# Optimization experiments

Measured on AMD Instinct MI355X. Metric: run time of the kernel, lower is better.

## Reference

```python
import jax, jax.numpy as jnp
import numpy as np

N = 20000        # nodes per type
E = 320000       # edges per type (avg degree 16)
H = 8            # heads
F0 = 128         # initial feature dim
F_UNI = 256      # n_unified
F_OUT = 64       # n_units per layer
N_USER = 20000   # shape_ret[0]
N_CLASSES = 2


def setup_inputs() -> dict:
    key = jax.random.key(0)
    ks = jax.random.split(key, 32)
    nrm = lambda k, s: jax.random.normal(k, s, dtype=jnp.float32) * 0.05
    inp = {
        "hemb0": nrm(ks[0], (N, F0)),
        "hemb1": nrm(ks[1], (N, F0)),
        "W0": nrm(ks[2], (F0, F_UNI)),
        "W1": nrm(ks[3], (F0, F_UNI)),
    }
    i = 4
    for t in range(2):
        for l, fin in enumerate([F_UNI, H * F_OUT]):
            inp[f"g{t}l{l}_w"] = nrm(ks[i], (H, fin, F_OUT)); i += 1
            inp[f"g{t}l{l}_asrc"] = nrm(ks[i], (H, F_OUT)); i += 1
            inp[f"g{t}l{l}_atrg"] = nrm(ks[i], (H, F_OUT)); i += 1
    inp["aw1"] = nrm(ks[i], (F_UNI, F_OUT)); i += 1
    inp["aw2"] = nrm(ks[i], (F_OUT, F_OUT)); i += 1
    inp["am"] = nrm(ks[i], (F_OUT,)); i += 1
    inp["fc_w"] = nrm(ks[i], (F_OUT * 3, N_CLASSES)); i += 1
    inp["fc_b"] = jnp.zeros((N_CLASSES,), jnp.float32); i += 1
    inp["edge0"] = jax.random.randint(ks[i], (2, E), 0, N, dtype=jnp.int32); i += 1
    inp["edge1"] = jax.random.randint(ks[i], (2, E), 0, N, dtype=jnp.int32)
    return inp


def spgat(h, src, trg, w, asrc, atrg):
    """Sparse GAT layer: h [N,f_in], edge list src/trg [E] -> [N,H,f_out]."""
    n = h.shape[0]
    hp = jnp.einsum('nf,hfo->hno', h, w)              # [H,N,O]
    s = jnp.einsum('hno,ho->nh', hp, asrc)            # [N,H]
    t = jnp.einsum('hno,ho->nh', hp, atrg)            # [N,H]
    e = jax.nn.leaky_relu(s[src] + t[trg], negative_slope=0.2)  # [E,H]
    ex = jnp.exp(e - jnp.max(e))                      # global max shift (as in source)
    denom = jax.ops.segment_sum(ex, trg, num_segments=n)[trg] + 1e-16
    alpha = ex / denom                                # [E,H]
    msg = jnp.transpose(hp, (1, 0, 2))[src] * alpha[:, :, None]  # [E,H,O]
    return jax.ops.segment_sum(msg, trg, num_segments=n)         # [N,H,O]


def reference(hemb0, hemb1, W0, W1,
              g0l0_w, g0l0_asrc, g0l0_atrg, g0l1_w, g0l1_asrc, g0l1_atrg,
              g1l0_w, g1l0_asrc, g1l0_atrg, g1l1_w, g1l1_asrc, g1l1_atrg,
              aw1, aw2, am, fc_w, fc_b, edge0, edge1):
    trans0 = hemb0 @ W0                                # [N,F_UNI]
    trans1 = hemb1 @ W1
    stacks = [
        (trans0, edge0, (g0l0_w, g0l0_asrc, g0l0_atrg), (g0l1_w, g0l1_asrc, g0l1_atrg)),
        (trans1, edge1, (g1l0_w, g1l0_asrc, g1l0_atrg), (g1l1_w, g1l1_asrc, g1l1_atrg)),
    ]
    heter = []
    for trans, edge, p0, p1 in stacks:
        src, trg = edge[0], edge[1]
        x = spgat(trans, src, trg, *p0)                # [N,H,F_OUT]
        x = jax.nn.elu(x.reshape(N, -1))               # [N,H*F_OUT]
        x = spgat(x, src, trg, *p1).mean(axis=1)       # [N,F_OUT]
        heter.append(x[:N_USER][:, None, :])
    type_aware = jnp.concatenate(heter, axis=1)        # [N_USER, 2, F_OUT]
    # faithful to source: feature = trans_emb[0] where trans_emb is the LAST
    # type's transformed embedding -> row 0, shape [F_UNI], broadcast over nodes
    feature = trans1[0]
    q = jnp.tanh(feature @ aw1 + type_aware @ aw2)     # [N_USER,2,F_OUT]
    beta = jax.nn.softmax(q @ am, axis=-1)             # [N_USER,2]
    fusion = jnp.einsum('nr,nrd->nd', beta, type_aware)[:, None, :]
    ret = jnp.concatenate([type_aware, fusion], axis=1).reshape(N_USER, -1)
    return jax.nn.log_softmax(ret @ fc_w + fc_b, axis=-1)   # [N_USER, 2]
```

## Files before the change

### kernel.cpp

```cpp
#include <hip/hip_runtime.h>
#include <hip/hip_bf16.h>


typedef __hip_bfloat16 bf16;
typedef __attribute__((ext_vector_type(8))) short short8;
typedef __attribute__((ext_vector_type(4))) float f32x4;

__device__ __forceinline__ float bf2f(bf16 v) { return __bfloat162float(v); }
__device__ __forceinline__ float ldin(const void* p, long i, int f32) {
  return f32 ? ((const float*)p)[i] : bf2f(((const bf16*)p)[i]);
}
__device__ __forceinline__ short f2bfbits(float f) {
  bf16 h = __float2bfloat16(f);
  return *reinterpret_cast<short*>(&h);
}
__device__ __forceinline__ float bfbits2f(short b) {
  unsigned u = ((unsigned)(unsigned short)b) << 16;
  return __uint_as_float(u);
}

struct GArg {
  const void* A[2];
  const void* B[2];
  bf16* C[2];
  const void* sa[2];
  const void* sb[2];
  float* sv[2];
  float* tv[2];
};

struct AArg {
  const bf16* hp[2];
  const float* sv[2];
  const float* tv[2];
  const int* rp[2];
  const int* col[2];
  void* out[2];
};

__global__ __launch_bounds__(64) void detect_kernel(const void* __restrict__ x,
                                                    int* __restrict__ flag) {
  int tid = threadIdx.x;
  float m = 0.f;
  for (int i = tid; i < 2048; i += 64) {
    float v = fabsf(bf2f(((const bf16*)x)[i]));
    if (!(v <= 1e3f)) v = 1e9f;
    m = fmaxf(m, v);
  }
#pragma unroll
  for (int off = 32; off; off >>= 1) m = fmaxf(m, __shfl_xor(m, off));
  if (tid == 0) flag[0] = (m > 1e3f) ? 1 : 0;
}

__global__ __launch_bounds__(256) void tr_kernel(const bf16* __restrict__ wg,
                                                 bf16* __restrict__ wgT,
                                                 const void* __restrict__ gw1a,
                                                 const void* __restrict__ gw1b,
                                                 bf16* __restrict__ bt1,
                                                 const int* __restrict__ flag) {
  const int f32 = flag[0];
  long i = (long)blockIdx.x * 256 + threadIdx.x;
  const long nW = 2L * 512 * 128;
  const long nB = 2L * 512 * 512;
  if (i < nW) {
    int t = (int)(i >> 16);
    long r = i & 65535;
    int c = (int)(r >> 7), k = (int)(r & 127);
    wgT[i] = wg[(long)t * 65536 + (long)k * 512 + c];
  } else if (i < nW + nB) {
    long r = i - nW;
    int t = (int)(r >> 18);
    long q = r & 262143;
    int c = (int)(q >> 9), k = (int)(q & 511);
    const void* g = t ? gw1b : gw1a;
    float v = ldin(g, ((long)(c >> 6) * 512 + k) * 64 + (c & 63), f32);
    bt1[r] = __float2bfloat16(v);
  }
}

#define GBM 128
#define GBN 64
#define GBK 64

__device__ __forceinline__ int swz(int row, int kbyte) {
  return row * 128 + (kbyte ^ ((row & 7) << 4));
}

__global__ __launch_bounds__(256) void gemm_mfma(GArg g, int amode, int bmode,
                                                 int M, int K, int Nc,
                                                 const int* __restrict__ flag) {
  __shared__ bf16 As[GBM * GBK];
  __shared__ bf16 Bs[GBN * GBK];
  const int z = blockIdx.z;
  const void* __restrict__ A = g.A[z];
  const void* __restrict__ B = g.B[z];
  bf16* __restrict__ C = g.C[z];
  const void* stasrc = g.sa[z];
  const void* statrg = g.sb[z];
  float* svp = g.sv[z];
  float* tvp = g.tv[z];
  const int f32 = flag[0];
  const int af32 = (amode == 1) ? f32 : 0;
  const int bf32 = (bmode == 2 || bmode == 3) ? 0 : f32;

  const int nx = gridDim.x >> 3;
  const int d = blockIdx.x;
  const int fullC = (gridDim.x >> 6) << 6;
  int x, y;
  if (d < fullC) {
    x = (d & 7) + ((d >> 6) << 3);
    y = (d >> 3) & 7;
  } else {
    int l = d - fullC;
    int xbase = fullC >> 3;
    int nrem = nx - xbase;
    x = xbase + l % nrem;
    y = l / nrem;
  }
  const int m0 = x * GBM;
  const int n0 = y * GBN;
  const int tid = threadIdx.x;
  const int lane = tid & 63;
  const int wrow = (tid >> 6) * 32;

  f32x4 acc[2][4];
#pragma unroll
  for (int m = 0; m < 2; m++)
#pragma unroll
    for (int n = 0; n < 4; n++)
#pragma unroll
      for (int r = 0; r < 4; r++) acc[m][n][r] = 0.f;

  for (int kt = 0; kt < K; kt += GBK) {
#pragma unroll
    for (int j = 0; j < 4; j++) {
      int idx = tid + j * 256;
      int row = idx >> 3;
      int ks = idx & 7;
      int gm = m0 + row;
      short8 v;
#pragma unroll
      for (int e = 0; e < 8; e++) v[e] = 0;
      if (gm < M) {
        long base = (long)gm * K + kt + ks * 8;
        if (!af32) {
          v = *(const short8*)((const bf16*)A + base);
        } else {
          const float* Af = (const float*)A + base;
          float4 x0 = *(const float4*)Af;
          float4 x1 = *(const float4*)(Af + 4);
          v[0] = f2bfbits(x0.x); v[1] = f2bfbits(x0.y);
          v[2] = f2bfbits(x0.z); v[3] = f2bfbits(x0.w);
          v[4] = f2bfbits(x1.x); v[5] = f2bfbits(x1.y);
          v[6] = f2bfbits(x1.z); v[7] = f2bfbits(x1.w);
        }
      }
      *(short8*)((char*)As + swz(row, ks * 16)) = v;
    }
    if (bmode == 3) {
      const bf16* BT = (const bf16*)B;
#pragma unroll
      for (int j = 0; j < 2; j++) {
        int idx = tid + j * 256;
        int c = idx >> 3;
        int ks = idx & 7;
        short8 v = *(const short8*)(BT + (long)(n0 + c) * K + kt + ks * 8);
        *(short8*)((char*)Bs + swz(c, ks * 16)) = v;
      }
    } else {
      int n = tid & 63;
      int ks0 = tid >> 6;
#pragma unroll
      for (int jj = 0; jj < 2; jj++) {
        int ks = ks0 + jj * 4;
        int k = kt + ks * 8;
        int col = n0 + n;
        long base;
        int cstr;
        if (bmode == 1) { base = ((long)(col >> 6) * K + k) * 64 + (col & 63); cstr = 64; }
        else { base = (long)k * Nc + col; cstr = Nc; }
        short8 v;
        if (bf32) {
          const float* Bf = (const float*)B;
#pragma unroll
          for (int e = 0; e < 8; e++) v[e] = f2bfbits(Bf[base + (long)e * cstr]);
        } else {
          const bf16* Bh = (const bf16*)B;
#pragma unroll
          for (int e = 0; e < 8; e++) v[e] = *(const short*)&Bh[base + (long)e * cstr];
        }
        *(short8*)((char*)Bs + swz(n, ks * 16)) = v;
      }
    }
    __syncthreads();
#pragma unroll
    for (int kh = 0; kh < 2; kh++) {
      int klane = kh * 64 + ((lane >> 4) << 4);
      short8 af[2], bfr[4];
#pragma unroll
      for (int m = 0; m < 2; m++) {
        int row = wrow + m * 16 + (lane & 15);
        af[m] = *(const short8*)((const char*)As + swz(row, klane));
      }
#pragma unroll
      for (int n = 0; n < 4; n++) {
        int col = n * 16 + (lane & 15);
        bfr[n] = *(const short8*)((const char*)Bs + swz(col, klane));
      }
#pragma unroll
      for (int m = 0; m < 2; m++)
#pragma unroll
        for (int n = 0; n < 4; n++)
          acc[m][n] = __builtin_amdgcn_mfma_f32_16x16x32_bf16(af[m], bfr[n], acc[m][n], 0, 0, 0);
    }
    __syncthreads();
  }
  if (svp) {
    const int h = y;
    const int cl = lane & 15;
    float av[4], bv[4];
#pragma unroll
    for (int n = 0; n < 4; n++) {
      av[n] = ldin(stasrc, h * 64 + n * 16 + cl, f32);
      bv[n] = ldin(statrg, h * 64 + n * 16 + cl, f32);
    }
#pragma unroll
    for (int m = 0; m < 2; m++) {
#pragma unroll
      for (int r = 0; r < 4; r++) {
        float s = 0.f, t = 0.f;
#pragma unroll
        for (int n = 0; n < 4; n++) {
          s += acc[m][n][r] * av[n];
          t += acc[m][n][r] * bv[n];
        }
#pragma unroll
        for (int off = 1; off <= 8; off <<= 1) {
          s += __shfl_xor(s, off);
          t += __shfl_xor(t, off);
        }
        int row = m0 + wrow + m * 16 + ((lane >> 4) << 2) + r;
        if (cl == 0 && row < M) {
          svp[(long)row * 8 + h] = s;
          tvp[(long)row * 8 + h] = t;
        }
      }
    }
  }
#pragma unroll
  for (int m = 0; m < 2; m++) {
#pragma unroll
    for (int r = 0; r < 4; r++) {
      int row = m0 + wrow + m * 16 + ((lane >> 4) << 2) + r;
      if (row < M) {
#pragma unroll
        for (int n = 0; n < 4; n++) {
          int col = n0 + n * 16 + (lane & 15);
          C[(long)row * Nc + col] = __float2bfloat16(acc[m][n][r]);
        }
      }
    }
  }
}

#define FKBM 64

__device__ __forceinline__ int swz256(int row, int kbyte) {
  return row * 256 + (kbyte ^ ((row & 7) << 4));
}

__global__ __launch_bounds__(256) void gemm_fullk(GArg g, int M,
                                                  const int* __restrict__ flag) {
  __shared__ bf16 As[FKBM * 128];
  __shared__ bf16 Bs[64 * 128];
  const int z = blockIdx.z;
  const void* __restrict__ A = g.A[z];
  const bf16* __restrict__ BT = (const bf16*)g.B[z];
  bf16* __restrict__ C = g.C[z];
  const void* stasrc = g.sa[z];
  const void* statrg = g.sb[z];
  float* svp = g.sv[z];
  float* tvp = g.tv[z];
  const int f32 = flag[0];
  const int m0 = blockIdx.x * FKBM;
  const int tid = threadIdx.x;
  const int lane = tid & 63;
  const int wrow = (tid >> 6) * 16;

#pragma unroll
  for (int j = 0; j < 4; j++) {
    int idx = tid + j * 256;
    int row = idx >> 4;
    int ks = idx & 15;
    int gm = m0 + row;
    short8 v;
#pragma unroll
    for (int e = 0; e < 8; e++) v[e] = 0;
    if (gm < M) {
      long base = (long)gm * 128 + ks * 8;
      if (!f32) {
        v = *(const short8*)((const bf16*)A + base);
      } else {
        const float* Af = (const float*)A + base;
        float4 x0 = *(const float4*)Af;
        float4 x1 = *(const float4*)(Af + 4);
        v[0] = f2bfbits(x0.x); v[1] = f2bfbits(x0.y);
        v[2] = f2bfbits(x0.z); v[3] = f2bfbits(x0.w);
        v[4] = f2bfbits(x1.x); v[5] = f2bfbits(x1.y);
        v[6] = f2bfbits(x1.z); v[7] = f2bfbits(x1.w);
      }
    }
    *(short8*)((char*)As + swz256(row, ks * 16)) = v;
  }

  for (int p = 0; p < 8; p++) {
#pragma unroll
    for (int j = 0; j < 4; j++) {
      int idx = tid + j * 256;
      int c = idx >> 4;
      int ks = idx & 15;
      short8 v = *(const short8*)(BT + (long)(p * 64 + c) * 128 + ks * 8);
      *(short8*)((char*)Bs + swz256(c, ks * 16)) = v;
    }
    __syncthreads();
    f32x4 acc[4];
#pragma unroll
    for (int n = 0; n < 4; n++)
#pragma unroll
      for (int r = 0; r < 4; r++) acc[n][r] = 0.f;
#pragma unroll
    for (int kb = 0; kb < 4; kb++) {
      int klane = kb * 64 + ((lane >> 4) << 4);
      short8 af = *(const short8*)((const char*)As + swz256(wrow + (lane & 15), klane));
      short8 bfr[4];
#pragma unroll
      for (int n = 0; n < 4; n++)
        bfr[n] = *(const short8*)((const char*)Bs + swz256(n * 16 + (lane & 15), klane));
#pragma unroll
      for (int n = 0; n < 4; n++)
        acc[n] = __builtin_amdgcn_mfma_f32_16x16x32_bf16(af, bfr[n], acc[n], 0, 0, 0);
    }
    {
      const int cl = lane & 15;
      float av[4], bv[4];
#pragma unroll
      for (int n = 0; n < 4; n++) {
        av[n] = ldin(stasrc, p * 64 + n * 16 + cl, f32);
        bv[n] = ldin(statrg, p * 64 + n * 16 + cl, f32);
      }
#pragma unroll
      for (int r = 0; r < 4; r++) {
        float s = 0.f, t = 0.f;
#pragma unroll
        for (int n = 0; n < 4; n++) {
          s += acc[n][r] * av[n];
          t += acc[n][r] * bv[n];
        }
#pragma unroll
        for (int off = 1; off <= 8; off <<= 1) {
          s += __shfl_xor(s, off);
          t += __shfl_xor(t, off);
        }
        int row = m0 + wrow + ((lane >> 4) << 2) + r;
        if (cl == 0 && row < M) {
          svp[(long)row * 8 + p] = s;
          tvp[(long)row * 8 + p] = t;
        }
      }
    }
#pragma unroll
    for (int r = 0; r < 4; r++) {
      int row = m0 + wrow + ((lane >> 4) << 2) + r;
      if (row < M) {
#pragma unroll
        for (int n = 0; n < 4; n++) {
          int col = p * 64 + n * 16 + (lane & 15);
          C[(long)row * 512 + col] = __float2bfloat16(acc[n][r]);
        }
      }
    }
    __syncthreads();
  }
}

__global__ void hist2_kernel(const int* __restrict__ trg0, const int* __restrict__ trg1,
                             int* __restrict__ deg, int E, int N) {
  int e = blockIdx.x * 256 + threadIdx.x;
  if (e < E) atomicAdd(&deg[trg0[e]], 1);
  else if (e < 2 * E) atomicAdd(&deg[N + trg1[e - E]], 1);
}

__global__ __launch_bounds__(1024) void scan_kernel(const int* __restrict__ degb,
                                                    int* __restrict__ rpb,
                                                    int* __restrict__ filb, int N) {
  const int* deg = degb + (long)blockIdx.x * N;
  int* row_ptr = rpb + (long)blockIdx.x * (N + 1);
  int* fil = filb + (long)blockIdx.x * N;
  __shared__ int sums[1024];
  int tid = threadIdx.x;
  int chunk = (N + 1023) >> 10;
  int start = tid * chunk;
  int end = start + chunk;
  if (start > N) start = N;
  if (end > N) end = N;
  int s = 0;
  for (int i = start; i < end; i++) s += deg[i];
  sums[tid] = s;
  __syncthreads();
  for (int off = 1; off < 1024; off <<= 1) {
    int add = (tid >= off) ? sums[tid - off] : 0;
    __syncthreads();
    sums[tid] += add;
    __syncthreads();
  }
  int run = (tid > 0) ? sums[tid - 1] : 0;
  for (int i = start; i < end; i++) {
    row_ptr[i] = run;
    fil[i] = run;
    run += deg[i];
  }
  if (tid == 0) row_ptr[N] = sums[1023];
}

__global__ void fill2_kernel(const int* __restrict__ src0, const int* __restrict__ trg0,
                             const int* __restrict__ src1, const int* __restrict__ trg1,
                             int* __restrict__ filb, int* __restrict__ colb, int E, int N) {
  int e = blockIdx.x * 256 + threadIdx.x;
  if (e < E) {
    int t = trg0[e];
    int pos = atomicAdd(&filb[t], 1);
    colb[pos] = src0[e];
  } else if (e < 2 * E) {
    int ee = e - E;
    int t = trg1[ee];
    int pos = atomicAdd(&filb[N + t], 1);
    colb[E + pos] = src1[ee];
  }
}

__device__ __forceinline__ float exleaky(float v) {
  v = v > 0.f ? v : 0.2f * v;
  return __expf(v);
}

__global__ __launch_bounds__(256) void aggregate(AArg aa, int N, int mode) {
  const int ty = blockIdx.y;
  const bf16* __restrict__ hpb = aa.hp[ty];
  const float* __restrict__ svb = aa.sv[ty];
  const float* __restrict__ tvb = aa.tv[ty];
  const int* __restrict__ rp = aa.rp[ty];
  const int* __restrict__ colv = aa.col[ty];
  void* __restrict__ outp = aa.out[ty];
  const int wid = threadIdx.x >> 6;
  const int lane = threadIdx.x & 63;
  const int n = blockIdx.x * 4 + wid;
  if (n >= N) return;
  const int start = rp[n];
  const int deg = rp[n + 1] - start;
  const int h = lane >> 3;
  const float tvh = tvb[(long)n * 8 + h];
  const bf16* __restrict__ hpc = hpb + lane * 8;

  float acc[8] = {0.f, 0.f, 0.f, 0.f, 0.f, 0.f, 0.f, 0.f};
  float den = 1e-16f;

#define AG_LOAD(EB, V0, V1, V2, V3, Q0, Q1, Q2, Q3)                 \
  {                                                                 \
    int t0 = __shfl(mysrc, (EB) + 0), t1 = __shfl(mysrc, (EB) + 1); \
    int t2 = __shfl(mysrc, (EB) + 2), t3 = __shfl(mysrc, (EB) + 3); \
    V0 = *(const short8*)(hpc + (long)t0 * 512);                    \
    V1 = *(const short8*)(hpc + (long)t1 * 512);                    \
    V2 = *(const short8*)(hpc + (long)t2 * 512);                    \
    V3 = *(const short8*)(hpc + (long)t3 * 512);                    \
    Q0 = svb[(long)t0 * 8 + h];                                     \
    Q1 = svb[(long)t1 * 8 + h];                                     \
    Q2 = svb[(long)t2 * 8 + h];                                     \
    Q3 = svb[(long)t3 * 8 + h];                                     \
  }
#define AG_ACC(V0, V1, V2, V3, Q0, Q1, Q2, Q3)                      \
  {                                                                 \
    float a0 = exleaky(Q0 + tvh), a1 = exleaky(Q1 + tvh);           \
    float a2 = exleaky(Q2 + tvh), a3 = exleaky(Q3 + tvh);           \
    den += a0 + a1 + a2 + a3;                                       \
    _Pragma("unroll")                                               \
    for (int j = 0; j < 8; j++)                                     \
      acc[j] += a0 * bfbits2f(V0[j]) + a1 * bfbits2f(V1[j]) +       \
                a2 * bfbits2f(V2[j]) + a3 * bfbits2f(V3[j]);        \
  }

  for (int base = 0; base < deg; base += 64) {
    int cnt = deg - base;
    if (cnt > 64) cnt = 64;
    int mysrc = (lane < cnt) ? colv[start + base + lane] : 0;
    int nfull = cnt & ~3;
    if (nfull) {
      short8 v0, v1, v2, v3;
      float q0, q1, q2, q3;
      AG_LOAD(0, v0, v1, v2, v3, q0, q1, q2, q3);
      for (int e = 4; e < nfull; e += 4) {
        short8 w0 = v0, w1 = v1, w2 = v2, w3 = v3;
        float p0 = q0, p1 = q1, p2 = q2, p3 = q3;
        AG_LOAD(e, v0, v1, v2, v3, q0, q1, q2, q3);
        AG_ACC(w0, w1, w2, w3, p0, p1, p2, p3);
      }
      AG_ACC(v0, v1, v2, v3, q0, q1, q2, q3);
    }
    for (int e = nfull; e < cnt; e++) {
      int s0 = __shfl(mysrc, e);
      short8 v = *(const short8*)(hpc + (long)s0 * 512);
      float a = exleaky(svb[(long)s0 * 8 + h] + tvh);
      den += a;
#pragma unroll
      for (int j = 0; j < 8; j++) acc[j] += a * bfbits2f(v[j]);
    }
  }

  const float dinv = 1.f / den;
  if (mode == 0) {
    short8 o8;
#pragma unroll
    for (int j = 0; j < 8; j++) {
      float s = acc[j] * dinv;
      float ev = s > 0.f ? s : expm1f(s);
      o8[j] = f2bfbits(ev);
    }
    *(short8*)((bf16*)outp + (long)n * 512 + lane * 8) = o8;
  } else {
    float r[8];
#pragma unroll
    for (int j = 0; j < 8; j++) r[j] = acc[j] * dinv;
#pragma unroll
    for (int m = 8; m <= 32; m <<= 1)
#pragma unroll
      for (int j = 0; j < 8; j++) r[j] += __shfl_xor(r[j], m);
    if (lane < 8) {
      float* o = (float*)outp + (long)n * 128 + lane * 8;
#pragma unroll
      for (int j = 0; j < 8; j++) o[j] = r[j] * 0.125f;
    }
  }
}

__global__ __launch_bounds__(256) void favec2_kernel(const void* __restrict__ hemb1,
                                                     const void* __restrict__ W1,
                                                     const void* __restrict__ aw1,
                                                     float* __restrict__ favec,
                                                     const int* __restrict__ flag) {
  const int f32 = flag[0];
  __shared__ float s_h[128];
  __shared__ float s_r[256];
  __shared__ float part[4][64];
  const int tid = threadIdx.x;
  if (tid < 128) s_h[tid] = ldin(hemb1, tid, f32);
  __syncthreads();
  float r = 0.f;
  for (int i = 0; i < 128; i++) r += s_h[i] * ldin(W1, (long)i * 256 + tid, f32);
  s_r[tid] = r;
  __syncthreads();
  const int o = tid & 63;
  const int wv = tid >> 6;
  float acc = 0.f;
#pragma unroll
  for (int kk = 0; kk < 64; kk++) {
    int k = wv * 64 + kk;
    acc += s_r[k] * ldin(aw1, (long)k * 64 + o, f32);
  }
  part[wv][o] = acc;
  __syncthreads();
  if (tid < 64) favec[o] = part[0][o] + part[1][o] + part[2][o] + part[3][o];
}

#define FN 16
__global__ __launch_bounds__(256) void final_kernel(const float* __restrict__ ta,
                                                    const float* __restrict__ favec,
                                                    const void* __restrict__ aw2,
                                                    const void* __restrict__ am,
                                                    const void* __restrict__ fcw,
                                                    const void* __restrict__ fcb,
                                                    void* __restrict__ out, int N,
                                                    const int* __restrict__ flag) {
  const int f32 = flag[0];
  __shared__ float s_w[64 * 64];
  __shared__ float s_fc[384];
  __shared__ float s_misc[130];
  __shared__ float s_ta[FN * 128];
  const int tid = threadIdx.x;
  const int n0 = blockIdx.x * FN;
  for (int i = tid; i < 4096; i += 256) s_w[i] = ldin(aw2, i, f32);
  for (int i = tid; i < 384; i += 256) s_fc[i] = ldin(fcw, i, f32);
  if (tid < 64) s_misc[tid] = favec[tid];
  else if (tid < 128) s_misc[tid] = ldin(am, tid - 64, f32);
  else if (tid < 130) s_misc[tid] = ldin(fcb, tid - 128, f32);
  for (int idx = tid; idx < FN * 128; idx += 256) {
    int ni = idx >> 7;
    int j = idx & 127;
    int k = j >> 1, r = j & 1;
    int n = n0 + ni;
    s_ta[idx] = (n < N) ? ta[(long)n * 128 + r * 64 + k] : 0.f;
  }
  __syncthreads();
  const int o = tid & 63;
  const int wv = tid >> 6;
#pragma unroll
  for (int ni4 = 0; ni4 < 4; ni4++) {
    const int ni = wv * 4 + ni4;
    const int n = n0 + ni;
    if (n >= N) continue;
    const float* tb = &s_ta[ni * 128];
    float acc0 = s_misc[o], acc1 = acc0;
#pragma unroll 8
    for (int k = 0; k < 64; k++) {
      float2 t2 = *(const float2*)(tb + k * 2);
      float w = s_w[k * 64 + o];
      acc0 += t2.x * w;
      acc1 += t2.y * w;
    }
    float ta0 = tb[o * 2];
    float ta1 = tb[o * 2 + 1];
    float amv = s_misc[64 + o];
    float p0 = tanhf(acc0) * amv;
    float p1 = tanhf(acc1) * amv;
#pragma unroll
    for (int off = 32; off > 0; off >>= 1) {
      p0 += __shfl_xor(p0, off);
      p1 += __shfl_xor(p1, off);
    }
    float mx = fmaxf(p0, p1);
    float e0 = __expf(p0 - mx), e1 = __expf(p1 - mx);
    float b0 = e0 / (e0 + e1), b1 = e1 / (e0 + e1);
    float fus = b0 * ta0 + b1 * ta1;
    float l0 = ta0 * s_fc[o * 2 + 0] + ta1 * s_fc[(64 + o) * 2 + 0] + fus * s_fc[(128 + o) * 2 + 0];
    float l1 = ta0 * s_fc[o * 2 + 1] + ta1 * s_fc[(64 + o) * 2 + 1] + fus * s_fc[(128 + o) * 2 + 1];
#pragma unroll
    for (int off = 32; off > 0; off >>= 1) {
      l0 += __shfl_xor(l0, off);
      l1 += __shfl_xor(l1, off);
    }
    if (o == 0) {
      l0 += s_misc[128];
      l1 += s_misc[129];
      float m2 = fmaxf(l0, l1);
      float lse = m2 + logf(__expf(l0 - m2) + __expf(l1 - m2));
      if (f32) {
        ((float*)out)[n * 2 + 0] = l0 - lse;
        ((float*)out)[n * 2 + 1] = l1 - lse;
      } else {
        ((bf16*)out)[n * 2 + 0] = __float2bfloat16(l0 - lse);
        ((bf16*)out)[n * 2 + 1] = __float2bfloat16(l1 - lse);
      }
    }
  }
}

extern "C" void kernel_launch(void* const* d_in, const int* in_sizes, int n_in,
                              void* d_out, int out_size, void* d_ws, size_t ws_size,
                              hipStream_t stream) {
  constexpr int N = 20000, E = 320000, H = 8, F0 = 128, FU = 256, FO = 64;
  const void* hemb[2] = {d_in[0], d_in[1]};
  const void* W[2] = {d_in[2], d_in[3]};
  const void* gw[2][2] = {{d_in[4], d_in[7]}, {d_in[10], d_in[13]}};
  const void* gasrc[2][2] = {{d_in[5], d_in[8]}, {d_in[11], d_in[14]}};
  const void* gatrg[2][2] = {{d_in[6], d_in[9]}, {d_in[12], d_in[15]}};
  const void* aw1 = d_in[16];
  const void* aw2 = d_in[17];
  const void* am = d_in[18];
  const void* fcw = d_in[19];
  const void* fcb = d_in[20];
  const int* edge[2] = {(const int*)d_in[21], (const int*)d_in[22]};

  const size_t szWg = (size_t)F0 * 512 * 2;
  const size_t szWgT = szWg;
  const size_t szBT1 = (size_t)512 * 512 * 2;
  const size_t szHp = (size_t)N * 512 * 2;
  const size_t szSv = (size_t)N * 8 * 4;
  size_t need = 0;
  auto addsz = [&](size_t b) { need += (b + 255) & ~(size_t)255; };
  addsz(4);
  addsz(szWg * 2); addsz(szWgT * 2); addsz(szBT1 * 2);
  addsz(szHp * 2); addsz(szHp * 2);
  addsz(szSv * 2); addsz(szSv * 2);
  addsz((size_t)N * 128 * 4); addsz(256);
  addsz((size_t)2 * N * 4); addsz((size_t)2 * (N + 1) * 4);
  addsz((size_t)2 * N * 4); addsz((size_t)2 * E * 4);
  const bool batched = (ws_size >= need + 4096);
  const int TB = batched ? 2 : 1;

  char* p = (char*)d_ws;
  auto alloc = [&](size_t bytes) -> void* {
    void* r = (void*)p;
    p += (bytes + 255) & ~(size_t)255;
    return r;
  };
  int* flag = (int*)alloc(4);
  bf16* wg = (bf16*)alloc(szWg * 2);
  bf16* wgT = (bf16*)alloc(szWgT * 2);
  bf16* bt1 = (bf16*)alloc(szBT1 * 2);
  bf16* hp = (bf16*)alloc(szHp * TB);
  bf16* xbuf = (bf16*)alloc(szHp * TB);
  float* sv = (float*)alloc(szSv * TB);
  float* tv = (float*)alloc(szSv * TB);
  float* ta = (float*)alloc((size_t)N * 128 * 4);
  float* favec = (float*)alloc(256);
  int* degb = (int*)alloc((size_t)2 * N * 4);
  int* rpb = (int*)alloc((size_t)2 * (N + 1) * 4);
  int* filb = (int*)alloc((size_t)2 * N * 4);
  int* colb = (int*)alloc((size_t)2 * E * 4);

  detect_kernel<<<1, 64, 0, stream>>>(hemb[0], flag);

  hipMemsetAsync(degb, 0, (size_t)2 * N * 4, stream);
  hist2_kernel<<<(2 * E + 255) / 256, 256, 0, stream>>>(edge[0] + E, edge[1] + E, degb, E, N);
  scan_kernel<<<2, 1024, 0, stream>>>(degb, rpb, filb, N);
  fill2_kernel<<<(2 * E + 255) / 256, 256, 0, stream>>>(edge[0], edge[0] + E,
                                                        edge[1], edge[1] + E, filb, colb, E, N);

  favec2_kernel<<<1, 256, 0, stream>>>(hemb[1], W[1], aw1, favec, flag);

  {
    GArg gW{};
    for (int i = 0; i < 2; i++) {
      gW.A[i] = W[i]; gW.B[i] = gw[i][0]; gW.C[i] = wg + (size_t)i * F0 * 512;
      gW.sa[i] = nullptr; gW.sb[i] = nullptr; gW.sv[i] = nullptr; gW.tv[i] = nullptr;
    }
    gemm_mfma<<<dim3(8, 1, 2), 256, 0, stream>>>(gW, 1, 1, F0, FU, H * FO, flag);
  }

  tr_kernel<<<2560, 256, 0, stream>>>(wg, wgT, gw[0][1], gw[1][1], bt1, flag);

  const int gmx = (N + GBM - 1) / GBM;
  const int gfk = (N + FKBM - 1) / FKBM;
  const int npass = batched ? 1 : 2;
  const int TC = batched ? 2 : 1;

  auto hpP = [&](int b) { return hp + (size_t)b * N * 512; };
  auto xbufP = [&](int b) { return xbuf + (size_t)b * N * 512; };
  auto svP = [&](int b) { return sv + (size_t)b * N * 8; };
  auto tvP = [&](int b) { return tv + (size_t)b * N * 8; };

  for (int pass = 0; pass < npass; pass++) {
    int types[2] = {batched ? 0 : pass, batched ? 1 : pass};
    int bufs[2] = {0, batched ? 1 : 0};

    GArg g1{};
    for (int i = 0; i < TC; i++) {
      int t = types[i], b = bufs[i];
      g1.A[i] = hemb[t]; g1.B[i] = wgT + (size_t)t * 512 * 128; g1.C[i] = hpP(b);
      g1.sa[i] = gasrc[t][0]; g1.sb[i] = gatrg[t][0]; g1.sv[i] = svP(b); g1.tv[i] = tvP(b);
    }
    gemm_fullk<<<dim3(gfk, 1, TC), 256, 0, stream>>>(g1, N, flag);

    AArg a0{};
    for (int i = 0; i < TC; i++) {
      int t = types[i], b = bufs[i];
      a0.hp[i] = hpP(b); a0.sv[i] = svP(b); a0.tv[i] = tvP(b);
      a0.rp[i] = rpb + (size_t)t * (N + 1); a0.col[i] = colb + (size_t)t * E;
      a0.out[i] = xbufP(b);
    }
    aggregate<<<dim3((N + 3) / 4, TC), 256, 0, stream>>>(a0, N, 0);

    GArg g2{};
    for (int i = 0; i < TC; i++) {
      int t = types[i], b = bufs[i];
      g2.A[i] = xbufP(b); g2.B[i] = bt1 + (size_t)t * 512 * 512; g2.C[i] = hpP(b);
      g2.sa[i] = gasrc[t][1]; g2.sb[i] = gatrg[t][1]; g2.sv[i] = svP(b); g2.tv[i] = tvP(b);
    }
    gemm_mfma<<<dim3(gmx * 8, 1, TC), 256, 0, stream>>>(g2, 0, 3, N, H * FO, H * FO, flag);

    AArg a1{};
    for (int i = 0; i < TC; i++) {
      int t = types[i], b = bufs[i];
      a1.hp[i] = hpP(b); a1.sv[i] = svP(b); a1.tv[i] = tvP(b);
      a1.rp[i] = rpb + (size_t)t * (N + 1); a1.col[i] = colb + (size_t)t * E;
      a1.out[i] = ta + (size_t)t * FO;
    }
    aggregate<<<dim3((N + 3) / 4, TC), 256, 0, stream>>>(a1, N, 1);
  }

  final_kernel<<<(N + FN - 1) / FN, 256, 0, stream>>>(ta, favec, aw2, am, fcw, fcb, d_out, N, flag);
}
```

Before: 529.8 us.

## Split aggregation across heads and edges per wave with shuffle reduction

The aggregation kernel now launches one wave per (node, head) rather than one wave per node, with the head taken from a new grid dimension. The 64 lanes form 8 groups that each walk every eighth edge, then combine partial sums with xor-shuffles. The mean over heads in mode 1 becomes atomic adds into a buffer that is zeroed beforehand. This raises parallelism and spreads the per-node edge walk across lanes, at the cost of 8x more waves, gathers of only 128 bytes per edge, repeated index loads per head, and float atomics.

After: 1.118 ms. +111.1%, slower.

```diff
diff --git a/kernel.cpp b/kernel.cpp
--- a/kernel.cpp
+++ b/kernel.cpp
@@ -443,100 +443,83 @@
   return __expf(v);
 }
 
-__global__ __launch_bounds__(256) void aggregate(AArg aa, int N, int mode) {
-  const int ty = blockIdx.y;
+__global__ __launch_bounds__(256) void aggregate_h(AArg aa, int N, int mode) {
+  const int ty = blockIdx.z;
   const bf16* __restrict__ hpb = aa.hp[ty];
   const float* __restrict__ svb = aa.sv[ty];
   const float* __restrict__ tvb = aa.tv[ty];
   const int* __restrict__ rp = aa.rp[ty];
   const int* __restrict__ colv = aa.col[ty];
   void* __restrict__ outp = aa.out[ty];
+  const int h = blockIdx.y;
   const int wid = threadIdx.x >> 6;
   const int lane = threadIdx.x & 63;
   const int n = blockIdx.x * 4 + wid;
   if (n >= N) return;
   const int start = rp[n];
   const int deg = rp[n + 1] - start;
-  const int h = lane >> 3;
+  const int grp = lane >> 3;
+  const int il = lane & 7;
   const float tvh = tvb[(long)n * 8 + h];
-  const bf16* __restrict__ hpc = hpb + lane * 8;
+  const bf16* __restrict__ hpc = hpb + h * 64 + il * 8;
 
   float acc[8] = {0.f, 0.f, 0.f, 0.f, 0.f, 0.f, 0.f, 0.f};
-  float den = 1e-16f;
-
-#define AG_LOAD(EB, V0, V1, V2, V3, Q0, Q1, Q2, Q3)                 \
-  {                                                                 \
-    int t0 = __shfl(mysrc, (EB) + 0), t1 = __shfl(mysrc, (EB) + 1); \
-    int t2 = __shfl(mysrc, (EB) + 2), t3 = __shfl(mysrc, (EB) + 3); \
-    V0 = *(const short8*)(hpc + (long)t0 * 512);                    \
-    V1 = *(const short8*)(hpc + (long)t1 * 512);                    \
-    V2 = *(const short8*)(hpc + (long)t2 * 512);                    \
-    V3 = *(const short8*)(hpc + (long)t3 * 512);                    \
-    Q0 = svb[(long)t0 * 8 + h];                                     \
-    Q1 = svb[(long)t1 * 8 + h];                                     \
-    Q2 = svb[(long)t2 * 8 + h];                                     \
-    Q3 = svb[(long)t3 * 8 + h];                                     \
-  }
-#define AG_ACC(V0, V1, V2, V3, Q0, Q1, Q2, Q3)                      \
-  {                                                                 \
-    float a0 = exleaky(Q0 + tvh), a1 = exleaky(Q1 + tvh);           \
-    float a2 = exleaky(Q2 + tvh), a3 = exleaky(Q3 + tvh);           \
-    den += a0 + a1 + a2 + a3;                                       \
-    _Pragma("unroll")                                               \
-    for (int j = 0; j < 8; j++)                                     \
-      acc[j] += a0 * bfbits2f(V0[j]) + a1 * bfbits2f(V1[j]) +       \
-                a2 * bfbits2f(V2[j]) + a3 * bfbits2f(V3[j]);        \
-  }
+  float den = 0.f;
 
   for (int base = 0; base < deg; base += 64) {
     int cnt = deg - base;
     if (cnt > 64) cnt = 64;
-    int mysrc = (lane < cnt) ? colv[start + base + lane] : 0;
-    int nfull = cnt & ~3;
-    if (nfull) {
-      short8 v0, v1, v2, v3;
-      float q0, q1, q2, q3;
-      AG_LOAD(0, v0, v1, v2, v3, q0, q1, q2, q3);
-      for (int e = 4; e < nfull; e += 4) {
-        short8 w0 = v0, w1 = v1, w2 = v2, w3 = v3;
-        float p0 = q0, p1 = q1, p2 = q2, p3 = q3;
-        AG_LOAD(e, v0, v1, v2, v3, q0, q1, q2, q3);
-        AG_ACC(w0, w1, w2, w3, p0, p1, p2, p3);
-      }
-      AG_ACC(v0, v1, v2, v3, q0, q1, q2, q3);
-    }
-    for (int e = nfull; e < cnt; e++) {
+    int mysrc = 0;
+    float mysv = 0.f;
+    if (lane < cnt) {
+      mysrc = colv[start + base + lane];
+      mysv = svb[(long)mysrc * 8 + h];
+    }
+    int e = grp;
+    if (e < cnt) {
       int s0 = __shfl(mysrc, e);
-      short8 v = *(const short8*)(hpc + (long)s0 * 512);
-      float a = exleaky(svb[(long)s0 * 8 + h] + tvh);
+      float q0 = __shfl(mysv, e);
+      short8 v0 = *(const short8*)(hpc + (long)s0 * 512);
+      for (e += 8; e < cnt; e += 8) {
+        int s1 = __shfl(mysrc, e);
+        float q1 = __shfl(mysv, e);
+        short8 v1 = *(const short8*)(hpc + (long)s1 * 512);
+        float a = exleaky(q0 + tvh);
+        den += a;
+#pragma unroll
+        for (int j = 0; j < 8; j++) acc[j] += a * bfbits2f(v0[j]);
+        v0 = v1;
+        q0 = q1;
+      }
+      float a = exleaky(q0 + tvh);
       den += a;
 #pragma unroll
-      for (int j = 0; j < 8; j++) acc[j] += a * bfbits2f(v[j]);
-    }
-  }
-
-  const float dinv = 1.f / den;
-  if (mode == 0) {
-    short8 o8;
-#pragma unroll
-    for (int j = 0; j < 8; j++) {
-      float s = acc[j] * dinv;
-      float ev = s > 0.f ? s : expm1f(s);
-      o8[j] = f2bfbits(ev);
-    }
-    *(short8*)((bf16*)outp + (long)n * 512 + lane * 8) = o8;
-  } else {
-    float r[8];
-#pragma unroll
-    for (int j = 0; j < 8; j++) r[j] = acc[j] * dinv;
-#pragma unroll
-    for (int m = 8; m <= 32; m <<= 1)
-#pragma unroll
-      for (int j = 0; j < 8; j++) r[j] += __shfl_xor(r[j], m);
-    if (lane < 8) {
-      float* o = (float*)outp + (long)n * 128 + lane * 8;
-#pragma unroll
-      for (int j = 0; j < 8; j++) o[j] = r[j] * 0.125f;
+      for (int j = 0; j < 8; j++) acc[j] += a * bfbits2f(v0[j]);
+    }
+  }
+
+#pragma unroll
+  for (int m = 8; m <= 32; m <<= 1) {
+    den += __shfl_xor(den, m);
+#pragma unroll
+    for (int j = 0; j < 8; j++) acc[j] += __shfl_xor(acc[j], m);
+  }
+  const float dinv = 1.f / (den + 1e-16f);
+
+  if (grp == 0) {
+    if (mode == 0) {
+      short8 o8;
+#pragma unroll
+      for (int j = 0; j < 8; j++) {
+        float s = acc[j] * dinv;
+        float ev = s > 0.f ? s : expm1f(s);
+        o8[j] = f2bfbits(ev);
+      }
+      *(short8*)((bf16*)outp + (long)n * 512 + h * 64 + il * 8) = o8;
+    } else {
+      float* o = (float*)outp + (long)n * 128 + il * 8;
+#pragma unroll
+      for (int j = 0; j < 8; j++) atomicAdd(&o[j], acc[j] * dinv * 0.125f);
     }
   }
 }
@@ -714,6 +697,8 @@
   fill2_kernel<<<(2 * E + 255) / 256, 256, 0, stream>>>(edge[0], edge[0] + E,
                                                         edge[1], edge[1] + E, filb, colb, E, N);
 
+  hipMemsetAsync(ta, 0, (size_t)N * 128 * 4, stream);
+
   favec2_kernel<<<1, 256, 0, stream>>>(hemb[1], W[1], aw1, favec, flag);
 
   {
@@ -756,7 +741,7 @@
       a0.rp[i] = rpb + (size_t)t * (N + 1); a0.col[i] = colb + (size_t)t * E;
       a0.out[i] = xbufP(b);
     }
-    aggregate<<<dim3((N + 3) / 4, TC), 256, 0, stream>>>(a0, N, 0);
+    aggregate_h<<<dim3((N + 3) / 4, 8, TC), 256, 0, stream>>>(a0, N, 0);
 
     GArg g2{};
     for (int i = 0; i < TC; i++) {
@@ -773,7 +758,7 @@
       a1.rp[i] = rpb + (size_t)t * (N + 1); a1.col[i] = colb + (size_t)t * E;
       a1.out[i] = ta + (size_t)t * FO;
     }
-    aggregate<<<dim3((N + 3) / 4, TC), 256, 0, stream>>>(a1, N, 1);
+    aggregate_h<<<dim3((N + 3) / 4, 8, TC), 256, 0, stream>>>(a1, N, 1);
   }
 
   final_kernel<<<(N + FN - 1) / FN, 256, 0, stream>>>(ta, favec, aw2, am, fcw, fcb, d_out, N, flag);
```
